# Performance work log

Measured on AMD Instinct MI355X. Metric: run time of the kernel, lower is better.

The kernel has to match this reference:

```python
import jax, jax.numpy as jnp
import numpy as np

N_NODES = 10000
N_EDGES = 640000
F_IN = 128
HID = 128
F_OUT = 40
BN_EPS = 1e-5


def setup_inputs() -> dict:
    key = jax.random.key(0)
    ks = jax.random.split(key, 8)
    x = jax.random.normal(ks[0], (N_NODES, F_IN), dtype=jnp.float32)
    edge_row = jax.random.randint(ks[1], (N_EDGES,), 0, N_NODES)
    edge_col = jax.random.randint(ks[2], (N_EDGES,), 0, N_NODES)
    edge_val = jax.random.uniform(ks[3], (N_EDGES,), dtype=jnp.float32)
    W1 = jax.random.normal(ks[4], (F_IN, HID), dtype=jnp.float32) * 0.05
    W2 = jax.random.normal(ks[5], (HID, HID), dtype=jnp.float32) * 0.05
    W3 = jax.random.normal(ks[6], (HID, F_OUT), dtype=jnp.float32) * 0.05
    return {
        "x": x, "edge_row": edge_row, "edge_col": edge_col, "edge_val": edge_val,
        "W1": W1, "b1": jnp.zeros((HID,), jnp.float32),
        "gamma2": jnp.ones((HID,), jnp.float32), "beta2": jnp.zeros((HID,), jnp.float32),
        "W2": W2, "b2": jnp.zeros((HID,), jnp.float32),
        "gamma3": jnp.ones((HID,), jnp.float32), "beta3": jnp.zeros((HID,), jnp.float32),
        "W3": W3, "b3": jnp.zeros((F_OUT,), jnp.float32),
    }


def _spmm(edge_row, edge_col, edge_val, x, n_nodes):
    # out[i] = sum_{e: row[e]==i} val[e] * x[col[e]]  == torch.sparse.mm(adj, x)
    msgs = edge_val[:, None] * jnp.take(x, edge_col, axis=0)  # [E, F]
    return jax.ops.segment_sum(msgs, edge_row, num_segments=n_nodes)


def _batchnorm(x, gamma, beta):
    # BatchNorm1d (training-mode normalization, biased variance)
    mean = jnp.mean(x, axis=0)
    var = jnp.mean(jnp.square(x - mean), axis=0)
    return gamma * (x - mean) * jax.lax.rsqrt(var + BN_EPS) + beta


def reference(x, edge_row, edge_col, edge_val, W1, b1, gamma2, beta2,
              W2, b2, gamma3, beta3, W3, b3):
    n = x.shape[0]
    # layer 1: SpMM -> Linear -> ReLU -> (dropout=identity in eval) -> BN
    h = _spmm(edge_row, edge_col, edge_val, x, n)
    h = jax.nn.relu(h @ W1 + b1)
    h = _batchnorm(h, gamma2, beta2)
    # layer 2
    h = _spmm(edge_row, edge_col, edge_val, h, n)
    h = jax.nn.relu(h @ W2 + b2)
    h = _batchnorm(h, gamma3, beta3)
    # layer 3
    h = _spmm(edge_row, edge_col, edge_val, h, n)
    h = h @ W3 + b3
    return jax.nn.log_softmax(h, axis=1)
```

## Files before the change

### kernel.cpp

```cpp
#include <hip/hip_runtime.h>
#include <hip/hip_bf16.h>
#include <math.h>

#define N_NODES 10000
#define F 128
#define F_OUT_ 40
#define N_EDGES_ 640000
#define BN_EPS 1e-5f
#define NBIN 625
#define RPB 16
#define NWGA 64
#define EPW 10000
#define BINCAP 1536

__device__ __forceinline__ unsigned pack4(int col, float v) {
    __hip_bfloat16 b = __float2bfloat16(v);
    return ((unsigned)(*(unsigned short*)&b) << 16) | (unsigned)col;
}
__device__ __forceinline__ int   col_of(unsigned q) { return (int)(q & 0xFFFFu); }
__device__ __forceinline__ float val_of(unsigned q) { return __uint_as_float(q & 0xFFFF0000u); }
__device__ __forceinline__ float lo16f(unsigned w) { return __uint_as_float(w << 16); }
__device__ __forceinline__ float hi16f(unsigned w) { return __uint_as_float(w & 0xffff0000u); }

__global__ __launch_bounds__(256) void fused_g1h(const float* __restrict__ x,
        const float* __restrict__ W1, __hip_bfloat16* __restrict__ T,
        const int* __restrict__ erow, int* __restrict__ hist) {
    __shared__ float Ws[F * F];
    __shared__ float As[16][F];
    __shared__ int   lh[NBIN];
    int tid = threadIdx.x;
    if (blockIdx.x >= NBIN) {
        int w = blockIdx.x - NBIN;
        for (int t = tid; t < NBIN; t += 256) lh[t] = 0;
        __syncthreads();
        int e0 = w * EPW;
        for (int e = e0 + tid; e < e0 + EPW; e += 256)
            atomicAdd(&lh[erow[e] >> 4], 1);
        __syncthreads();
        for (int t = tid; t < NBIN; t += 256) hist[w * NBIN + t] = lh[t];
        return;
    }
    for (int i = tid; i < F * F; i += 256) Ws[i] = W1[i];
    int r0 = blockIdx.x * 16;
    for (int i = tid; i < 16 * F; i += 256) {
        int r2 = i >> 7, k = i & (F - 1);
        As[r2][k] = x[(size_t)(r0 + r2) * F + k];
    }
    __syncthreads();
    int c = tid & (F - 1), hh = tid >> 7;
    for (int r2 = hh; r2 < 16; r2 += 2) {
        float acc = 0.f;
        #pragma unroll
        for (int k = 0; k < F; ++k) acc = fmaf(As[r2][k], Ws[k * F + c], acc);
        T[(size_t)(r0 + r2) * F + c] = __float2bfloat16(acc);
    }
}

__global__ __launch_bounds__(64) void scan_w(const int* __restrict__ hist,
                                             int* __restrict__ offs,
                                             int* __restrict__ totals) {
    int b = blockIdx.x, t = threadIdx.x;
    int h = hist[t * NBIN + b];
    int v = h;
    #pragma unroll
    for (int off = 1; off < 64; off <<= 1) {
        int u = __shfl_up(v, off);
        if (t >= off) v += u;
    }
    offs[t * NBIN + b] = v - h;
    if (t == 63) totals[b] = v;
}

__global__ __launch_bounds__(1024) void scan_bins(const int* __restrict__ totals,
                                                  int* __restrict__ base) {
    __shared__ int sc[1024];
    int tid = threadIdx.x;
    int val = (tid < NBIN) ? totals[tid] : 0;
    sc[tid] = val;
    __syncthreads();
    for (int off = 1; off < 1024; off <<= 1) {
        int v = 0;
        if (tid >= off) v = sc[tid - off];
        __syncthreads();
        if (tid >= off) sc[tid] += v;
        __syncthreads();
    }
    if (tid < NBIN) base[tid] = sc[tid] - val;
    if (tid == NBIN - 1) base[NBIN] = sc[tid];
}

__global__ __launch_bounds__(1024) void scatter_bin(const int* __restrict__ erow,
                                                    const int* __restrict__ ecol,
                                                    const float* __restrict__ eval_,
                                                    const int* __restrict__ offs,
                                                    const int* __restrict__ base,
                                                    int2* __restrict__ ebin) {
    __shared__ int myoff[NBIN];
    __shared__ int cur[NBIN];
    int w = blockIdx.x, tid = threadIdx.x;
    for (int t = tid; t < NBIN; t += 1024) {
        myoff[t] = base[t] + offs[w * NBIN + t];
        cur[t] = 0;
    }
    __syncthreads();
    int e0 = w * EPW, e1 = e0 + EPW;
    int e = e0 + tid;
    for (; e + 3072 < e1; e += 4096) {
        int   r0 = erow[e],        r1 = erow[e + 1024],  r2 = erow[e + 2048],  r3 = erow[e + 3072];
        int   c0 = ecol[e],        c1 = ecol[e + 1024],  c2 = ecol[e + 2048],  c3 = ecol[e + 3072];
        float v0 = eval_[e],       v1 = eval_[e + 1024], v2 = eval_[e + 2048], v3 = eval_[e + 3072];
        int b0 = r0 >> 4, b1 = r1 >> 4, b2 = r2 >> 4, b3 = r3 >> 4;
        int p0 = atomicAdd(&cur[b0], 1);
        int p1 = atomicAdd(&cur[b1], 1);
        int p2 = atomicAdd(&cur[b2], 1);
        int p3 = atomicAdd(&cur[b3], 1);
        ebin[myoff[b0] + p0] = make_int2((r0 << 14) | c0, __float_as_int(v0));
        ebin[myoff[b1] + p1] = make_int2((r1 << 14) | c1, __float_as_int(v1));
        ebin[myoff[b2] + p2] = make_int2((r2 << 14) | c2, __float_as_int(v2));
        ebin[myoff[b3] + p3] = make_int2((r3 << 14) | c3, __float_as_int(v3));
    }
    for (; e < e1; e += 1024) {
        int r = erow[e];
        int b = r >> 4;
        int p = atomicAdd(&cur[b], 1);
        ebin[myoff[b] + p] = make_int2((r << 14) | ecol[e], __float_as_int(eval_[e]));
    }
}

__global__ __launch_bounds__(256) void sort_bin(const int* __restrict__ base,
                                                const int2* __restrict__ ebin,
                                                unsigned* __restrict__ ebin2,
                                                int* __restrict__ rowptr) {
    __shared__ int2    ein[BINCAP];
    __shared__ unsigned eout[BINCAP];
    __shared__ int cnt16[16], pos16[16], exc[16];
    int b = blockIdx.x, tid = threadIdx.x;
    int lo = base[b], hi = base[b + 1];
    int n = min(hi - lo, BINCAP);
    for (int i = tid; i < n; i += 256) ein[i] = ebin[lo + i];
    if (tid < 16) cnt16[tid] = 0;
    __syncthreads();
    for (int i = tid; i < n; i += 256)
        atomicAdd(&cnt16[(ein[i].x >> 14) & 15], 1);
    __syncthreads();
    if (tid == 0) {
        int run = 0;
        #pragma unroll
        for (int j = 0; j < 16; ++j) { exc[j] = run; run += cnt16[j]; }
    }
    __syncthreads();
    if (tid < 16) {
        pos16[tid] = exc[tid];
        rowptr[b * RPB + tid] = lo + exc[tid];
    }
    if (b == NBIN - 1 && tid == 0) rowptr[N_NODES] = hi;
    __syncthreads();
    for (int i = tid; i < n; i += 256) {
        int2 q = ein[i];
        int j = (q.x >> 14) & 15;
        int p = atomicAdd(&pos16[j], 1);
        eout[p] = pack4(q.x & 16383, __int_as_float(q.y));
    }
    __syncthreads();
    for (int i = tid; i < n; i += 256) ebin2[lo + i] = eout[i];
}

__global__ __launch_bounds__(256) void spmm_row4(const int* __restrict__ rowptr,
                                                 const unsigned* __restrict__ epk,
                                                 const uint2* __restrict__ T2,
                                                 float* __restrict__ Z,
                                                 float* __restrict__ accs) {
    if (blockIdx.x == 0 && threadIdx.x < 256) accs[threadIdx.x] = 0.f;
    int wv = threadIdx.x >> 6, lane = threadIdx.x & 63;
    int r = blockIdx.x * 4 + wv;
    if (r >= N_NODES) return;
    int beg = rowptr[r], end = rowptr[r + 1];
    int half = lane >> 5, l2 = lane & 31;
    float a0c0 = 0.f, a0c1 = 0.f, a1c0 = 0.f, a1c1 = 0.f;
    float a2c0 = 0.f, a2c1 = 0.f, a3c0 = 0.f, a3c1 = 0.f;
    for (int bb = beg; bb < end; bb += 64) {
        int m = min(end - bb, 64);
        unsigned myq = (lane < m) ? epk[bb + lane] : 0u;
        int j = 0;
        for (; j + 16 <= m; j += 16) {
            unsigned q[8]; uint2 w[8];
            #pragma unroll
            for (int t = 0; t < 8; ++t) {
                q[t] = __shfl(myq, j + 2 * t + half);
                w[t] = T2[(unsigned)col_of(q[t]) * 32u + l2];
            }
            #pragma unroll
            for (int t = 0; t < 8; ++t) {
                float v = val_of(q[t]);
                if (t & 1) {
                    a0c1 = fmaf(v, lo16f(w[t].x), a0c1);
                    a1c1 = fmaf(v, hi16f(w[t].x), a1c1);
                    a2c1 = fmaf(v, lo16f(w[t].y), a2c1);
                    a3c1 = fmaf(v, hi16f(w[t].y), a3c1);
                } else {
                    a0c0 = fmaf(v, lo16f(w[t].x), a0c0);
                    a1c0 = fmaf(v, hi16f(w[t].x), a1c0);
                    a2c0 = fmaf(v, lo16f(w[t].y), a2c0);
                    a3c0 = fmaf(v, hi16f(w[t].y), a3c0);
                }
            }
        }
        for (; j + 2 <= m; j += 2) {
            unsigned q = __shfl(myq, j + half);
            uint2 w = T2[(unsigned)col_of(q) * 32u + l2];
            float v = val_of(q);
            a0c0 = fmaf(v, lo16f(w.x), a0c0);
            a1c0 = fmaf(v, hi16f(w.x), a1c0);
            a2c0 = fmaf(v, lo16f(w.y), a2c0);
            a3c0 = fmaf(v, hi16f(w.y), a3c0);
        }
        if (j < m) {
            unsigned q = __shfl(myq, j);
            uint2 w = T2[(unsigned)col_of(q) * 32u + l2];
            float v = half ? 0.f : val_of(q);
            a0c0 = fmaf(v, lo16f(w.x), a0c0);
            a1c0 = fmaf(v, hi16f(w.x), a1c0);
            a2c0 = fmaf(v, lo16f(w.y), a2c0);
            a3c0 = fmaf(v, hi16f(w.y), a3c0);
        }
    }
    float a0 = a0c0 + a0c1, a1 = a1c0 + a1c1;
    float a2 = a2c0 + a2c1, a3 = a3c0 + a3c1;
    a0 += __shfl_xor(a0, 32);
    a1 += __shfl_xor(a1, 32);
    a2 += __shfl_xor(a2, 32);
    a3 += __shfl_xor(a3, 32);
    if (half == 0) {
        float4 o = make_float4(a0, a1, a2, a3);
        *(float4*)(Z + (size_t)r * F + 4 * l2) = o;
    }
}

__global__ __launch_bounds__(256) void spmm40_ls(const int* __restrict__ rowptr,
                                                 const unsigned* __restrict__ epk,
                                                 const unsigned short* __restrict__ T40,
                                                 const float* __restrict__ b3,
                                                 float* __restrict__ out) {
    int wv = threadIdx.x >> 6, lane = threadIdx.x & 63;
    int w = blockIdx.x * 4 + wv;
    if (w >= N_NODES) return;
    int beg = rowptr[w], end = rowptr[w + 1];
    float a[4] = {0.f, 0.f, 0.f, 0.f};
    const unsigned short* Tb = T40 + lane;
    bool act = (lane < F_OUT_);
    for (int base = beg; base < end; base += 64) {
        int m = min(end - base, 64);
        unsigned myq = 0;
        if (lane < m) myq = epk[base + lane];
        int j = 0;
        for (; j + 8 <= m; j += 8) {
            unsigned q[8];
            #pragma unroll
            for (int t = 0; t < 8; ++t) q[t] = __shfl(myq, j + t);
            if (act) {
                unsigned short u[8];
                #pragma unroll
                for (int t = 0; t < 8; ++t) u[t] = Tb[(unsigned)col_of(q[t]) * 40u];
                #pragma unroll
                for (int t = 0; t < 8; ++t)
                    a[t & 3] = fmaf(val_of(q[t]),
                                    __uint_as_float(((unsigned)u[t]) << 16), a[t & 3]);
            }
        }
        for (; j < m; ++j) {
            unsigned q = __shfl(myq, j);
            if (act) {
                unsigned short u = Tb[(unsigned)col_of(q) * 40u];
                a[0] = fmaf(val_of(q), __uint_as_float(((unsigned)u) << 16), a[0]);
            }
        }
    }
    float acc = (a[0] + a[1]) + (a[2] + a[3]);
    float val = act ? acc + b3[lane] : -INFINITY;
    float m2 = val;
    #pragma unroll
    for (int off = 32; off > 0; off >>= 1) m2 = fmaxf(m2, __shfl_xor(m2, off));
    float e = act ? expf(val - m2) : 0.f;
    float s = e;
    #pragma unroll
    for (int off = 32; off > 0; off >>= 1) s += __shfl_xor(s, off);
    if (act) out[(size_t)w * F_OUT_ + lane] = val - m2 - logf(s);
}


__global__ void bn_stats_br(const float* __restrict__ X, const float* __restrict__ bias,
                            float* __restrict__ acc) {
    int f = threadIdx.x & (F - 1);
    float b = bias[f];
    float s = 0.f, s2 = 0.f;
    long long total = (long long)N_NODES * F;
    long long stride = (long long)gridDim.x * blockDim.x;
    for (long long idx = (long long)blockIdx.x * blockDim.x + threadIdx.x;
         idx < total; idx += stride) {
        float t = fmaxf(X[idx] + b, 0.f);
        s += t; s2 += t * t;
    }
    __shared__ float ls[256], ls2[256];
    ls[threadIdx.x] = s; ls2[threadIdx.x] = s2;
    __syncthreads();
    if (threadIdx.x < 128) {
        s  = ls[threadIdx.x] + ls[threadIdx.x + 128];
        s2 = ls2[threadIdx.x] + ls2[threadIdx.x + 128];
        atomicAdd(&acc[f], s);
        atomicAdd(&acc[F + f], s2);
    }
}


__global__ __launch_bounds__(256) void gemm128_bn(const float* __restrict__ A,
        const float* __restrict__ W, const float* __restrict__ bias,
        const float* __restrict__ gamma, const float* __restrict__ beta,
        const float* __restrict__ accs, __hip_bfloat16* __restrict__ C) {
    __shared__ float Ws[F * F];
    __shared__ float As[16][F];
    __shared__ float sc[F], sh[F], bi[F];
    int tid = threadIdx.x;
    if (tid < F) {
        float m   = accs[tid] / (float)N_NODES;
        float var = accs[F + tid] / (float)N_NODES - m * m;
        float rs  = rsqrtf(var + BN_EPS);
        float g   = gamma[tid] * rs;
        sc[tid] = g;
        sh[tid] = beta[tid] - g * m;
        bi[tid] = bias[tid];
    }
    for (int i = tid; i < F * F; i += 256) Ws[i] = W[i];
    __syncthreads();
    int r0 = blockIdx.x * 16;
    for (int i = tid; i < 16 * F; i += 256) {
        int r2 = i >> 7, k = i & (F - 1);
        float a = A[(size_t)(r0 + r2) * F + k];
        As[r2][k] = fmaxf(a + bi[k], 0.f) * sc[k] + sh[k];
    }
    __syncthreads();
    int c = tid & (F - 1), hh = tid >> 7;
    for (int r2 = hh; r2 < 16; r2 += 2) {
        float acc = 0.f;
        #pragma unroll
        for (int k = 0; k < F; ++k) acc = fmaf(As[r2][k], Ws[k * F + c], acc);
        C[(size_t)(r0 + r2) * F + c] = __float2bfloat16(acc);
    }
}

__global__ __launch_bounds__(256) void gemm40_bn(const float* __restrict__ A,
        const float* __restrict__ W, const float* __restrict__ bias,
        const float* __restrict__ gamma, const float* __restrict__ beta,
        const float* __restrict__ accs, __hip_bfloat16* __restrict__ C) {
    __shared__ float Ws[F * F_OUT_];
    __shared__ float sc[F], sh[F], bi[F];
    int tid = threadIdx.x;
    if (tid < F) {
        float m   = accs[tid] / (float)N_NODES;
        float var = accs[F + tid] / (float)N_NODES - m * m;
        float rs  = rsqrtf(var + BN_EPS);
        float g   = gamma[tid] * rs;
        sc[tid] = g;
        sh[tid] = beta[tid] - g * m;
        bi[tid] = bias[tid];
    }
    for (int i = tid; i < F * F_OUT_; i += 256) Ws[i] = W[i];
    __syncthreads();
    int c = tid % F_OUT_, rl = tid / F_OUT_;
    if (rl >= 6) return;
    int r = blockIdx.x * 6 + rl;
    if (r >= N_NODES) return;
    const float* a = A + (size_t)r * F;
    float acc = 0.f;
    #pragma unroll
    for (int k = 0; k < F; ++k) {
        float t = fmaxf(a[k] + bi[k], 0.f) * sc[k] + sh[k];
        acc = fmaf(t, Ws[k * F_OUT_ + c], acc);
    }
    C[(size_t)r * F_OUT_ + c] = __float2bfloat16(acc);
}


extern "C" void kernel_launch(void* const* d_in, const int* in_sizes, int n_in,
                              void* d_out, int out_size, void* d_ws, size_t ws_size,
                              hipStream_t stream) {
    const float* x      = (const float*)d_in[0];
    const int*   erow   = (const int*)  d_in[1];
    const int*   ecol   = (const int*)  d_in[2];
    const float* eval_  = (const float*)d_in[3];
    const float* W1     = (const float*)d_in[4];
    const float* b1     = (const float*)d_in[5];
    const float* gamma2 = (const float*)d_in[6];
    const float* beta2  = (const float*)d_in[7];
    const float* W2     = (const float*)d_in[8];
    const float* b2     = (const float*)d_in[9];
    const float* gamma3 = (const float*)d_in[10];
    const float* beta3  = (const float*)d_in[11];
    const float* W3     = (const float*)d_in[12];
    const float* b3     = (const float*)d_in[13];
    float* out = (float*)d_out;

    const size_t nf = (size_t)N_NODES * F;
    const int BLK = 256;

    int*   hist   = (int*)d_ws;
    int*   offs   = hist + NWGA * NBIN;
    int*   totals = offs + NWGA * NBIN;
    int*   base   = totals + 640;
    float* accs   = (float*)(base + 640);
    int*   rowptr = (int*)(accs + 256);
    __hip_bfloat16* T = (__hip_bfloat16*)(rowptr + 10016);
    float* Z     = (float*)((char*)T + nf * 2);
    int2*  ebin  = (int2*)(Z + nf);
    unsigned* ebin2 = (unsigned*)(ebin + N_EDGES_);

    fused_g1h<<<NBIN + NWGA, BLK, 0, stream>>>(x, W1, T, erow, hist);
    scan_w<<<NBIN, 64, 0, stream>>>(hist, offs, totals);
    scan_bins<<<1, 1024, 0, stream>>>(totals, base);
    scatter_bin<<<NWGA, 1024, 0, stream>>>(erow, ecol, eval_, offs, base, ebin);
    sort_bin<<<NBIN, BLK, 0, stream>>>(base, ebin, ebin2, rowptr);

    const int GB4 = (N_NODES + 3) / 4;

    spmm_row4<<<GB4, BLK, 0, stream>>>(rowptr, ebin2, (const uint2*)T, Z, accs);
    bn_stats_br<<<256, BLK, 0, stream>>>(Z, b1, accs);

    gemm128_bn<<<NBIN, BLK, 0, stream>>>(Z, W2, b1, gamma2, beta2, accs, T);
    spmm_row4<<<GB4, BLK, 0, stream>>>(rowptr, ebin2, (const uint2*)T, Z, accs);
    bn_stats_br<<<256, BLK, 0, stream>>>(Z, b2, accs);

    gemm40_bn<<<(N_NODES + 5) / 6, BLK, 0, stream>>>(Z, W3, b2, gamma3, beta3, accs, T);
    spmm40_ls<<<GB4, BLK, 0, stream>>>(rowptr, ebin2, (const unsigned short*)T, b3, out);
}
```

Before: 151.1 us.

## Fuse BN statistics into SpMM and fold histogram scans into scatter

Removes the scan_w and scan_bins kernels by having each scatter_bin workgroup compute its own prefix offsets and global bin bases from the histogram directly. Removes the separate bn_stats_br passes by accumulating ReLU(Z+bias) sum and sum-of-squares per block in shared memory inside the SpMM, then atomically adding into one of eight replicated global accumulators that the GEMM kernels later reduce. This cuts four kernel launches and two full reads of Z, at the cost of redundant histogram reads per scatter workgroup and extra shared and global atomics in the SpMM.

New measurement: 149.9 us. About the same (-0.8%).

```diff
diff --git a/kernel.cpp b/kernel.cpp
--- a/kernel.cpp
+++ b/kernel.cpp
@@ -12,6 +12,7 @@
 #define NWGA 64
 #define EPW 10000
 #define BINCAP 1536
+#define NREP 8
 
 __device__ __forceinline__ unsigned pack4(int col, float v) {
     __hip_bfloat16 b = __float2bfloat16(v);
@@ -24,11 +25,15 @@
 
 __global__ __launch_bounds__(256) void fused_g1h(const float* __restrict__ x,
         const float* __restrict__ W1, __hip_bfloat16* __restrict__ T,
-        const int* __restrict__ erow, int* __restrict__ hist) {
+        const int* __restrict__ erow, int* __restrict__ hist,
+        float* __restrict__ accsZ ) {
     __shared__ float Ws[F * F];
     __shared__ float As[16][F];
     __shared__ int   lh[NBIN];
     int tid = threadIdx.x;
+    if (blockIdx.x == 0) {
+        for (int i = tid; i < 2 * NREP * 256; i += 256) accsZ[i] = 0.f;
+    }
     if (blockIdx.x >= NBIN) {
         int w = blockIdx.x - NBIN;
         for (int t = tid; t < NBIN; t += 256) lh[t] = 0;
@@ -56,26 +61,31 @@
     }
 }
 
-__global__ __launch_bounds__(64) void scan_w(const int* __restrict__ hist,
-                                             int* __restrict__ offs,
-                                             int* __restrict__ totals) {
-    int b = blockIdx.x, t = threadIdx.x;
-    int h = hist[t * NBIN + b];
-    int v = h;
-    #pragma unroll
-    for (int off = 1; off < 64; off <<= 1) {
-        int u = __shfl_up(v, off);
-        if (t >= off) v += u;
-    }
-    offs[t * NBIN + b] = v - h;
-    if (t == 63) totals[b] = v;
-}
-
-__global__ __launch_bounds__(1024) void scan_bins(const int* __restrict__ totals,
-                                                  int* __restrict__ base) {
+__global__ __launch_bounds__(1024) void scatter_bin(const int* __restrict__ erow,
+                                                    const int* __restrict__ ecol,
+                                                    const float* __restrict__ eval_,
+                                                    const int* __restrict__ hist,
+                                                    int* __restrict__ base_g,
+                                                    int2* __restrict__ ebin) {
+    __shared__ int myoff[NBIN];
+    __shared__ int tot[NBIN];
+    __shared__ int cur[NBIN];
     __shared__ int sc[1024];
-    int tid = threadIdx.x;
-    int val = (tid < NBIN) ? totals[tid] : 0;
+    int w = blockIdx.x, tid = threadIdx.x;
+    for (int b = tid; b < NBIN; b += 1024) {
+        int own = 0, all = 0;
+        #pragma unroll 8
+        for (int w2 = 0; w2 < NWGA; ++w2) {
+            int h = hist[w2 * NBIN + b];
+            all += h;
+            if (w2 < w) own += h;
+        }
+        myoff[b] = own;
+        tot[b] = all;
+        cur[b] = 0;
+    }
+    __syncthreads();
+    int val = (tid < NBIN) ? tot[tid] : 0;
     sc[tid] = val;
     __syncthreads();
     for (int off = 1; off < 1024; off <<= 1) {
@@ -85,23 +95,12 @@
         if (tid >= off) sc[tid] += v;
         __syncthreads();
     }
-    if (tid < NBIN) base[tid] = sc[tid] - val;
-    if (tid == NBIN - 1) base[NBIN] = sc[tid];
-}
-
-__global__ __launch_bounds__(1024) void scatter_bin(const int* __restrict__ erow,
-                                                    const int* __restrict__ ecol,
-                                                    const float* __restrict__ eval_,
-                                                    const int* __restrict__ offs,
-                                                    const int* __restrict__ base,
-                                                    int2* __restrict__ ebin) {
-    __shared__ int myoff[NBIN];
-    __shared__ int cur[NBIN];
-    int w = blockIdx.x, tid = threadIdx.x;
-    for (int t = tid; t < NBIN; t += 1024) {
-        myoff[t] = base[t] + offs[w * NBIN + t];
-        cur[t] = 0;
-    }
+    if (tid < NBIN) {
+        int base = sc[tid] - val;
+        myoff[tid] += base;
+        if (w == 0) base_g[tid] = base;
+    }
+    if (w == 0 && tid == 0) base_g[NBIN] = N_EDGES_;
     __syncthreads();
     int e0 = w * EPW, e1 = e0 + EPW;
     int e = e0 + tid;
@@ -165,15 +164,18 @@
     for (int i = tid; i < n; i += 256) ebin2[lo + i] = eout[i];
 }
 
-__global__ __launch_bounds__(256) void spmm_row4(const int* __restrict__ rowptr,
-                                                 const unsigned* __restrict__ epk,
-                                                 const uint2* __restrict__ T2,
-                                                 float* __restrict__ Z,
-                                                 float* __restrict__ accs) {
-    if (blockIdx.x == 0 && threadIdx.x < 256) accs[threadIdx.x] = 0.f;
-    int wv = threadIdx.x >> 6, lane = threadIdx.x & 63;
+__global__ __launch_bounds__(256) void spmm_row4s(const int* __restrict__ rowptr,
+                                                  const unsigned* __restrict__ epk,
+                                                  const uint2* __restrict__ T2,
+                                                  float* __restrict__ Z,
+                                                  const float* __restrict__ bias,
+                                                  float* __restrict__ accs) {
+    __shared__ float sacc[2][F];
+    int tid = threadIdx.x;
+    for (int i = tid; i < 2 * F; i += 256) ((float*)sacc)[i] = 0.f;
+    __syncthreads();
+    int wv = tid >> 6, lane = tid & 63;
     int r = blockIdx.x * 4 + wv;
-    if (r >= N_NODES) return;
     int beg = rowptr[r], end = rowptr[r + 1];
     int half = lane >> 5, l2 = lane & 31;
     float a0c0 = 0.f, a0c1 = 0.f, a1c0 = 0.f, a1c1 = 0.f;
@@ -231,8 +233,21 @@
     a2 += __shfl_xor(a2, 32);
     a3 += __shfl_xor(a3, 32);
     if (half == 0) {
-        float4 o = make_float4(a0, a1, a2, a3);
-        *(float4*)(Z + (size_t)r * F + 4 * l2) = o;
+        *(float4*)(Z + (size_t)r * F + 4 * l2) = make_float4(a0, a1, a2, a3);
+        float4 bi = *(const float4*)(bias + 4 * l2);
+        float t0 = fmaxf(a0 + bi.x, 0.f), t1 = fmaxf(a1 + bi.y, 0.f);
+        float t2 = fmaxf(a2 + bi.z, 0.f), t3 = fmaxf(a3 + bi.w, 0.f);
+        atomicAdd(&sacc[0][4 * l2],     t0); atomicAdd(&sacc[1][4 * l2],     t0 * t0);
+        atomicAdd(&sacc[0][4 * l2 + 1], t1); atomicAdd(&sacc[1][4 * l2 + 1], t1 * t1);
+        atomicAdd(&sacc[0][4 * l2 + 2], t2); atomicAdd(&sacc[1][4 * l2 + 2], t2 * t2);
+        atomicAdd(&sacc[0][4 * l2 + 3], t3); atomicAdd(&sacc[1][4 * l2 + 3], t3 * t3);
+    }
+    __syncthreads();
+    int rep = blockIdx.x & (NREP - 1);
+    float* dst = accs + rep * 2 * F;
+    for (int i = tid; i < F; i += 256) {
+        atomicAdd(&dst[i],     sacc[0][i]);
+        atomicAdd(&dst[F + i], sacc[1][i]);
     }
 }
 
@@ -288,30 +303,6 @@
 }
 
 
-__global__ void bn_stats_br(const float* __restrict__ X, const float* __restrict__ bias,
-                            float* __restrict__ acc) {
-    int f = threadIdx.x & (F - 1);
-    float b = bias[f];
-    float s = 0.f, s2 = 0.f;
-    long long total = (long long)N_NODES * F;
-    long long stride = (long long)gridDim.x * blockDim.x;
-    for (long long idx = (long long)blockIdx.x * blockDim.x + threadIdx.x;
-         idx < total; idx += stride) {
-        float t = fmaxf(X[idx] + b, 0.f);
-        s += t; s2 += t * t;
-    }
-    __shared__ float ls[256], ls2[256];
-    ls[threadIdx.x] = s; ls2[threadIdx.x] = s2;
-    __syncthreads();
-    if (threadIdx.x < 128) {
-        s  = ls[threadIdx.x] + ls[threadIdx.x + 128];
-        s2 = ls2[threadIdx.x] + ls2[threadIdx.x + 128];
-        atomicAdd(&acc[f], s);
-        atomicAdd(&acc[F + f], s2);
-    }
-}
-
-
 __global__ __launch_bounds__(256) void gemm128_bn(const float* __restrict__ A,
         const float* __restrict__ W, const float* __restrict__ bias,
         const float* __restrict__ gamma, const float* __restrict__ beta,
@@ -321,8 +312,14 @@
     __shared__ float sc[F], sh[F], bi[F];
     int tid = threadIdx.x;
     if (tid < F) {
-        float m   = accs[tid] / (float)N_NODES;
-        float var = accs[F + tid] / (float)N_NODES - m * m;
+        float s = 0.f, s2 = 0.f;
+        #pragma unroll
+        for (int rp = 0; rp < NREP; ++rp) {
+            s  += accs[rp * 2 * F + tid];
+            s2 += accs[rp * 2 * F + F + tid];
+        }
+        float m   = s / (float)N_NODES;
+        float var = s2 / (float)N_NODES - m * m;
         float rs  = rsqrtf(var + BN_EPS);
         float g   = gamma[tid] * rs;
         sc[tid] = g;
@@ -355,8 +352,14 @@
     __shared__ float sc[F], sh[F], bi[F];
     int tid = threadIdx.x;
     if (tid < F) {
-        float m   = accs[tid] / (float)N_NODES;
-        float var = accs[F + tid] / (float)N_NODES - m * m;
+        float s = 0.f, s2 = 0.f;
+        #pragma unroll
+        for (int rp = 0; rp < NREP; ++rp) {
+            s  += accs[rp * 2 * F + tid];
+            s2 += accs[rp * 2 * F + F + tid];
+        }
+        float m   = s / (float)N_NODES;
+        float var = s2 / (float)N_NODES - m * m;
         float rs  = rsqrtf(var + BN_EPS);
         float g   = gamma[tid] * rs;
         sc[tid] = g;
@@ -403,31 +406,26 @@
     const int BLK = 256;
 
     int*   hist   = (int*)d_ws;
-    int*   offs   = hist + NWGA * NBIN;
-    int*   totals = offs + NWGA * NBIN;
-    int*   base   = totals + 640;
-    float* accs   = (float*)(base + 640);
-    int*   rowptr = (int*)(accs + 256);
+    int*   base_g = hist + NWGA * NBIN;
+    float* accsA  = (float*)(base_g + 626);
+    float* accsB  = accsA + NREP * 256;
+    int*   rowptr = (int*)(accsB + NREP * 256);
     __hip_bfloat16* T = (__hip_bfloat16*)(rowptr + 10016);
     float* Z     = (float*)((char*)T + nf * 2);
     int2*  ebin  = (int2*)(Z + nf);
     unsigned* ebin2 = (unsigned*)(ebin + N_EDGES_);
 
-    fused_g1h<<<NBIN + NWGA, BLK, 0, stream>>>(x, W1, T, erow, hist);
-    scan_w<<<NBIN, 64, 0, stream>>>(hist, offs, totals);
-    scan_bins<<<1, 1024, 0, stream>>>(totals, base);
-    scatter_bin<<<NWGA, 1024, 0, stream>>>(erow, ecol, eval_, offs, base, ebin);
-    sort_bin<<<NBIN, BLK, 0, stream>>>(base, ebin, ebin2, rowptr);
-
-    const int GB4 = (N_NODES + 3) / 4;
-
-    spmm_row4<<<GB4, BLK, 0, stream>>>(rowptr, ebin2, (const uint2*)T, Z, accs);
-    bn_stats_br<<<256, BLK, 0, stream>>>(Z, b1, accs);
-
-    gemm128_bn<<<NBIN, BLK, 0, stream>>>(Z, W2, b1, gamma2, beta2, accs, T);
-    spmm_row4<<<GB4, BLK, 0, stream>>>(rowptr, ebin2, (const uint2*)T, Z, accs);
-    bn_stats_br<<<256, BLK, 0, stream>>>(Z, b2, accs);
-
-    gemm40_bn<<<(N_NODES + 5) / 6, BLK, 0, stream>>>(Z, W3, b2, gamma3, beta3, accs, T);
+    fused_g1h<<<NBIN + NWGA, BLK, 0, stream>>>(x, W1, T, erow, hist, accsA);
+    scatter_bin<<<NWGA, 1024, 0, stream>>>(erow, ecol, eval_, hist, base_g, ebin);
+    sort_bin<<<NBIN, BLK, 0, stream>>>(base_g, ebin, ebin2, rowptr);
+
+    const int GB4 = N_NODES / 4;
+
+    spmm_row4s<<<GB4, BLK, 0, stream>>>(rowptr, ebin2, (const uint2*)T, Z, b1, accsA);
+
+    gemm128_bn<<<NBIN, BLK, 0, stream>>>(Z, W2, b1, gamma2, beta2, accsA, T);
+    spmm_row4s<<<GB4, BLK, 0, stream>>>(rowptr, ebin2, (const uint2*)T, Z, b2, accsB);
+
+    gemm40_bn<<<(N_NODES + 5) / 6, BLK, 0, stream>>>(Z, W3, b2, gamma3, beta3, accsB, T);
     spmm40_ls<<<GB4, BLK, 0, stream>>>(rowptr, ebin2, (const unsigned short*)T, b3, out);
 }
```
